# Optimization experiments

Measured on AMD Instinct MI355X. Metric: run time of the kernel, lower is better.

Reference implementation:

```python
import jax, jax.numpy as jnp
import numpy as np

N_NODES = 100000
N_EDGES = 1600000
D = 128
EPS = 0.0  # train_eps=False -> constant


def setup_inputs() -> dict:
    key = jax.random.key(0)
    k = jax.random.split(key, 6)
    s = 1.0 / np.sqrt(D)
    return {
        "X": jax.random.normal(k[0], (N_NODES, D), dtype=jnp.float32),
        "W1": jax.random.normal(k[1], (D, D), dtype=jnp.float32) * s,
        "b1": jnp.zeros((D,), dtype=jnp.float32),
        "W2": jax.random.normal(k[2], (D, D), dtype=jnp.float32) * s,
        "b2": jnp.zeros((D,), dtype=jnp.float32),
        "edge_src": jax.random.randint(k[3], (N_EDGES,), 0, N_NODES, dtype=jnp.int32),
        "edge_dst": jax.random.randint(k[4], (N_EDGES,), 0, N_NODES, dtype=jnp.int32),
    }


def reference(X, W1, b1, W2, b2, edge_src, edge_dst):
    # v2v sum aggregation: agg[i] = sum_{j in N(i)} X[j]
    msgs = X[edge_src]  # (E, D) gather
    agg = jax.ops.segment_sum(msgs, edge_dst, num_segments=N_NODES)  # (N, D)
    h = (1.0 + EPS) * X + agg
    # MLP: Linear -> ReLU -> Linear
    h = jax.nn.relu(h @ W1 + b1)
    out = h @ W2 + b2
    return out
```

## Files before the change

### kernel.cpp

```cpp
#include <hip/hip_runtime.h>
#include <hip/hip_bf16.h>

#define N_NODES 100000
#define N_EDGES 1600000
#define D 128

#define NBINS 196
#define BINSHIFT 9
#define BINCAP 10000
#define EPB 8192

typedef __bf16 bf16x8 __attribute__((ext_vector_type(8)));
typedef short short8 __attribute__((ext_vector_type(8)));
typedef float f32x4 __attribute__((ext_vector_type(4)));

__device__ __forceinline__ unsigned short f2bf(float f) {
  union { float f; unsigned u; } c; c.f = f;
  unsigned u = c.u;
  u += 0x7FFFu + ((u >> 16) & 1u);
  return (unsigned short)(u >> 16);
}
__device__ __forceinline__ float bflo(unsigned u) {
  union { unsigned u; float f; } c; c.u = u << 16; return c.f;
}
__device__ __forceinline__ float bfhi(unsigned u) {
  union { unsigned u; float f; } c; c.u = u & 0xFFFF0000u; return c.f;
}


__launch_bounds__(512)
__global__ void k_bin(const int* __restrict__ esrc, const int* __restrict__ edst,
                      int* __restrict__ g_bincnt, uint2* __restrict__ binbuf) {
  __shared__ int cnt[NBINS];
  __shared__ int base[NBINS];
  const int t = threadIdx.x;
  const int e0 = blockIdx.x * EPB;
  const int ne = min(EPB, N_EDGES - e0);
  for (int i = t; i < NBINS; i += 512) cnt[i] = 0;
  __syncthreads();
  for (int i = t; i < ne; i += 512)
    atomicAdd(&cnt[edst[e0 + i] >> BINSHIFT], 1);
  __syncthreads();
  for (int i = t; i < NBINS; i += 512) {
    base[i] = atomicAdd(&g_bincnt[i], cnt[i]);
    cnt[i] = 0;
  }
  __syncthreads();
  for (int i = t; i < ne; i += 512) {
    int d = edst[e0 + i];
    int s = esrc[e0 + i];
    int b = d >> BINSHIFT;
    int pos = base[b] + atomicAdd(&cnt[b], 1);
    binbuf[(size_t)b * BINCAP + pos] = make_uint2((unsigned)s, (unsigned)d);
  }
}

__global__ void k_binscan(const int* __restrict__ g_bincnt, int* __restrict__ binstart) {
  __shared__ int s[256];
  int t = threadIdx.x;
  int v = (t < NBINS) ? g_bincnt[t] : 0;
  s[t] = v;
  __syncthreads();
  for (int d = 1; d < 256; d <<= 1) {
    int x = (t >= d) ? s[t - d] : 0;
    __syncthreads();
    s[t] += x;
    __syncthreads();
  }
  if (t < NBINS) binstart[t] = s[t] - v;
}

__launch_bounds__(512)
__global__ void k_binsort(const uint2* __restrict__ binbuf, const int* __restrict__ g_bincnt,
                          const int* __restrict__ binstart, int* __restrict__ srt,
                          int* __restrict__ deg, int* __restrict__ offs) {
  __shared__ int hist[512];
  __shared__ int scan[512];
  const int b = blockIdx.x, t = threadIdx.x;
  const int cnt = g_bincnt[b];
  const int n0 = b << BINSHIFT;
  const int gbase = binstart[b];
  const uint2* eb = binbuf + (size_t)b * BINCAP;

  hist[t] = 0;
  __syncthreads();
  for (int i = t; i < cnt; i += 512)
    atomicAdd(&hist[eb[i].y - n0], 1);
  __syncthreads();
  int v = hist[t];
  scan[t] = v;
  __syncthreads();
  for (int d = 1; d < 512; d <<= 1) {
    int x = (t >= d) ? scan[t - d] : 0;
    __syncthreads();
    scan[t] += x;
    __syncthreads();
  }
  int n = n0 + t;
  if (n < N_NODES) {
    deg[n] = v;
    offs[n] = gbase + scan[t] - v;
  }
  hist[t] = scan[t] - v;
  __syncthreads();
  for (int i = t; i < cnt; i += 512) {
    uint2 e = eb[i];
    int pos = atomicAdd(&hist[e.y - n0], 1);
    srt[gbase + pos] = (int)e.x;
  }
}


__global__ void k_hist(const int* __restrict__ dst, int* __restrict__ deg) {
  int i = blockIdx.x * 256 + threadIdx.x;
  if (i < N_EDGES) atomicAdd(&deg[dst[i]], 1);
}

__global__ void k_scan1(const int* __restrict__ deg, int* __restrict__ offs,
                        int* __restrict__ bsum) {
  __shared__ int s[1024];
  int t = threadIdx.x;
  int i = blockIdx.x * 1024 + t;
  int v = (i < N_NODES) ? deg[i] : 0;
  s[t] = v;
  __syncthreads();
  for (int d = 1; d < 1024; d <<= 1) {
    int x = (t >= d) ? s[t - d] : 0;
    __syncthreads();
    s[t] += x;
    __syncthreads();
  }
  if (i < N_NODES) offs[i] = s[t] - v;
  if (t == 1023) bsum[blockIdx.x] = s[t];
}

__global__ void k_scan2(int* __restrict__ bsum) {
  __shared__ int s[128];
  int t = threadIdx.x;
  int v = (t < 98) ? bsum[t] : 0;
  s[t] = v;
  __syncthreads();
  for (int d = 1; d < 128; d <<= 1) {
    int x = (t >= d) ? s[t - d] : 0;
    __syncthreads();
    s[t] += x;
    __syncthreads();
  }
  if (t < 98) bsum[t] = s[t] - v;
}

__global__ void k_scan3(int* __restrict__ offs, const int* __restrict__ bsum) {
  int i = blockIdx.x * 1024 + threadIdx.x;
  if (i < N_NODES) offs[i] += bsum[blockIdx.x];
}

__global__ void k_bucket(const int* __restrict__ src, const int* __restrict__ dst,
                         int* __restrict__ offs, int* __restrict__ srt) {
  int i = blockIdx.x * 256 + threadIdx.x;
  if (i < N_EDGES) {
    int pos = atomicAdd(&offs[dst[i]], 1);
    srt[pos] = src[i];
  }
}

__global__ void k_cvt(const float* __restrict__ X, unsigned short* __restrict__ Xb) {
  size_t i = (size_t)(blockIdx.x * 256 + threadIdx.x) * 8;
  const float4* p = (const float4*)(X + i);
  float4 a = p[0], b = p[1];
  short8 s;
  s[0] = f2bf(a.x); s[1] = f2bf(a.y); s[2] = f2bf(a.z); s[3] = f2bf(a.w);
  s[4] = f2bf(b.x); s[5] = f2bf(b.y); s[6] = f2bf(b.z); s[7] = f2bf(b.w);
  *(short8*)(Xb + i) = s;
}

__global__ void k_gather_bf(const unsigned int* __restrict__ X1,
                            const int* __restrict__ deg, const int* __restrict__ offs,
                            const int* __restrict__ srt, unsigned int* __restrict__ h0) {
  int node = blockIdx.x * 4 + (threadIdx.x >> 6);
  int lane = threadIdx.x & 63;
  unsigned u = X1[(size_t)node * 64 + lane];
  float hx = bflo(u), hy = bfhi(u);
  int e = offs[node];
  int end = e + deg[node];
  for (; e + 8 <= end; e += 8) {
    int s0 = srt[e],     s1 = srt[e + 1], s2 = srt[e + 2], s3 = srt[e + 3];
    int s4 = srt[e + 4], s5 = srt[e + 5], s6 = srt[e + 6], s7 = srt[e + 7];
    unsigned u0 = X1[(size_t)s0 * 64 + lane];
    unsigned u1 = X1[(size_t)s1 * 64 + lane];
    unsigned u2 = X1[(size_t)s2 * 64 + lane];
    unsigned u3 = X1[(size_t)s3 * 64 + lane];
    unsigned u4 = X1[(size_t)s4 * 64 + lane];
    unsigned u5 = X1[(size_t)s5 * 64 + lane];
    unsigned u6 = X1[(size_t)s6 * 64 + lane];
    unsigned u7 = X1[(size_t)s7 * 64 + lane];
    hx += bflo(u0); hy += bfhi(u0);
    hx += bflo(u1); hy += bfhi(u1);
    hx += bflo(u2); hy += bfhi(u2);
    hx += bflo(u3); hy += bfhi(u3);
    hx += bflo(u4); hy += bfhi(u4);
    hx += bflo(u5); hy += bfhi(u5);
    hx += bflo(u6); hy += bfhi(u6);
    hx += bflo(u7); hy += bfhi(u7);
  }
  for (; e + 2 <= end; e += 2) {
    unsigned u0 = X1[(size_t)srt[e] * 64 + lane];
    unsigned u1 = X1[(size_t)srt[e + 1] * 64 + lane];
    hx += bflo(u0); hy += bfhi(u0);
    hx += bflo(u1); hy += bfhi(u1);
  }
  for (; e < end; ++e) {
    unsigned u0 = X1[(size_t)srt[e] * 64 + lane];
    hx += bflo(u0); hy += bfhi(u0);
  }
  h0[(size_t)node * 64 + lane] = ((unsigned)f2bf(hy) << 16) | f2bf(hx);
}

__global__ void k_gather(const float* __restrict__ X, const int* __restrict__ deg,
                         const int* __restrict__ offs, const int* __restrict__ srt,
                         float* __restrict__ out) {
  int node = blockIdx.x * 4 + (threadIdx.x >> 6);
  int lane = threadIdx.x & 63;
  const float2* X2 = (const float2*)X;
  float2 h = X2[(size_t)node * 64 + lane];
  int end = offs[node];
  int dg = deg[node];
  for (int e = end - dg; e < end; ++e) {
    int s = srt[e];
    float2 x = X2[(size_t)s * 64 + lane];
    h.x += x.x; h.y += x.y;
  }
  ((float2*)out)[(size_t)node * 64 + lane] = h;
}

#define BR 256
#define PADK 136

template <bool BF>
__launch_bounds__(512, 1)
__global__ void k_mlp(const void* __restrict__ h0v,
                      const float* __restrict__ W1, const float* __restrict__ b1,
                      const float* __restrict__ W2, const float* __restrict__ b2,
                      float* __restrict__ out) {
  __shared__ __attribute__((aligned(16))) unsigned short lW1[128 * PADK];
  __shared__ __attribute__((aligned(16))) unsigned short lW2[128 * PADK];
  __shared__ __attribute__((aligned(16))) unsigned short lH[BR * PADK];

  const int t = threadIdx.x;
  const int wave = t >> 6, lane = t & 63;
  const int lr = lane & 15, lg = lane >> 4;
  const int row0 = blockIdx.x * BR;
  const int wrow = row0 + wave * 32;

  for (int i = t; i < 128 * 128; i += 512) {
    int k = i >> 7, n = i & 127;
    lW1[n * PADK + k] = f2bf(W1[i]);
    lW2[n * PADK + k] = f2bf(W2[i]);
  }

  bf16x8 a[2][4];
#pragma unroll
  for (int tr = 0; tr < 2; ++tr) {
#pragma unroll
    for (int kb = 0; kb < 4; ++kb) {
      int r = wrow + tr * 16 + lr;
      if (r >= N_NODES) r = N_NODES - 1;
      if constexpr (BF) {
        const unsigned short* h0 = (const unsigned short*)h0v;
        a[tr][kb] = __builtin_bit_cast(bf16x8,
            *(const short8*)(h0 + (size_t)r * D + kb * 32 + lg * 8));
      } else {
        const float* h0 = (const float*)h0v;
        const float4* p = (const float4*)(h0 + (size_t)r * D + kb * 32 + lg * 8);
        float4 f0 = p[0], f1 = p[1];
        short8 s;
        s[0] = f2bf(f0.x); s[1] = f2bf(f0.y); s[2] = f2bf(f0.z); s[3] = f2bf(f0.w);
        s[4] = f2bf(f1.x); s[5] = f2bf(f1.y); s[6] = f2bf(f1.z); s[7] = f2bf(f1.w);
        a[tr][kb] = __builtin_bit_cast(bf16x8, s);
      }
    }
  }

  f32x4 acc[2][8];
#pragma unroll
  for (int nc = 0; nc < 8; ++nc) {
    float bb = b1[nc * 16 + lr];
#pragma unroll
    for (int tr = 0; tr < 2; ++tr) acc[tr][nc] = (f32x4){bb, bb, bb, bb};
  }

  __syncthreads();

#pragma unroll
  for (int nc = 0; nc < 8; ++nc) {
#pragma unroll
    for (int kb = 0; kb < 4; ++kb) {
      bf16x8 b = *(const bf16x8*)&lW1[(nc * 16 + lr) * PADK + kb * 32 + lg * 8];
#pragma unroll
      for (int tr = 0; tr < 2; ++tr)
        acc[tr][nc] = __builtin_amdgcn_mfma_f32_16x16x32_bf16(a[tr][kb], b, acc[tr][nc], 0, 0, 0);
    }
  }

#pragma unroll
  for (int tr = 0; tr < 2; ++tr) {
#pragma unroll
    for (int nc = 0; nc < 8; ++nc) {
#pragma unroll
      for (int r = 0; r < 4; ++r) {
        float v = acc[tr][nc][r];
        v = v > 0.f ? v : 0.f;
        int lrow = wave * 32 + tr * 16 + lg * 4 + r;
        lH[lrow * PADK + nc * 16 + lr] = f2bf(v);
      }
    }
  }

  __syncthreads();

  bf16x8 a2[2][4];
#pragma unroll
  for (int tr = 0; tr < 2; ++tr) {
#pragma unroll
    for (int kb = 0; kb < 4; ++kb)
      a2[tr][kb] = *(const bf16x8*)&lH[(wave * 32 + tr * 16 + lr) * PADK + kb * 32 + lg * 8];
  }

#pragma unroll
  for (int nc = 0; nc < 8; ++nc) {
    float bb = b2[nc * 16 + lr];
#pragma unroll
    for (int tr = 0; tr < 2; ++tr) acc[tr][nc] = (f32x4){bb, bb, bb, bb};
  }

#pragma unroll
  for (int nc = 0; nc < 8; ++nc) {
#pragma unroll
    for (int kb = 0; kb < 4; ++kb) {
      bf16x8 b = *(const bf16x8*)&lW2[(nc * 16 + lr) * PADK + kb * 32 + lg * 8];
#pragma unroll
      for (int tr = 0; tr < 2; ++tr)
        acc[tr][nc] = __builtin_amdgcn_mfma_f32_16x16x32_bf16(a2[tr][kb], b, acc[tr][nc], 0, 0, 0);
    }
  }

#pragma unroll
  for (int tr = 0; tr < 2; ++tr) {
#pragma unroll
    for (int nc = 0; nc < 8; ++nc) {
#pragma unroll
      for (int r = 0; r < 4; ++r) {
        int row = wrow + tr * 16 + lg * 4 + r;
        if (row < N_NODES) out[(size_t)row * D + nc * 16 + lr] = acc[tr][nc][r];
      }
    }
  }
}

extern "C" void kernel_launch(void* const* d_in, const int* in_sizes, int n_in,
                              void* d_out, int out_size, void* d_ws, size_t ws_size,
                              hipStream_t stream) {
  const float* X  = (const float*)d_in[0];
  const float* W1 = (const float*)d_in[1];
  const float* b1 = (const float*)d_in[2];
  const float* W2 = (const float*)d_in[3];
  const float* b2 = (const float*)d_in[4];
  const int* esrc = (const int*)d_in[5];
  const int* edst = (const int*)d_in[6];
  float* out = (float*)d_out;

  char* ws = (char*)d_ws;
  int* deg      = (int*)(ws);
  int* offs     = (int*)(ws + 400000);
  int* g_bincnt = (int*)(ws + 800000);
  int* binstart = (int*)(ws + 801024);
  int* srt      = (int*)(ws + 802048);
  unsigned short* Xb  = (unsigned short*)(ws + 7202048);
  unsigned short* h0b = (unsigned short*)(ws + 32802048);
  uint2* binbuf = (uint2*)(ws + 32802048);
  const size_t NEED = 58402048;

  if (ws_size >= NEED) {
    hipMemsetAsync(g_bincnt, 0, NBINS * sizeof(int), stream);
    k_cvt      <<<(N_NODES * D) / (256 * 8), 256, 0, stream>>>(X, Xb);
    k_bin      <<<(N_EDGES + EPB - 1) / EPB, 512, 0, stream>>>(esrc, edst, g_bincnt, binbuf);
    k_binscan  <<<1, 256, 0, stream>>>(g_bincnt, binstart);
    k_binsort  <<<NBINS, 512, 0, stream>>>(binbuf, g_bincnt, binstart, srt, deg, offs);
    k_gather_bf<<<N_NODES / 4, 256, 0, stream>>>((const unsigned*)Xb, deg, offs, srt,
                                                 (unsigned*)h0b);
    k_mlp<true><<<(N_NODES + BR - 1) / BR, 512, 0, stream>>>(h0b, W1, b1, W2, b2, out);
  } else {
    int* bsum = g_bincnt;
    hipMemsetAsync(deg, 0, N_NODES * sizeof(int), stream);
    k_hist  <<<N_EDGES / 256, 256, 0, stream>>>(edst, deg);
    k_scan1 <<<98, 1024, 0, stream>>>(deg, offs, bsum);
    k_scan2 <<<1, 128, 0, stream>>>(bsum);
    k_scan3 <<<98, 1024, 0, stream>>>(offs, bsum);
    k_bucket<<<N_EDGES / 256, 256, 0, stream>>>(esrc, edst, offs, srt);
    k_gather<<<N_NODES / 4, 256, 0, stream>>>(X, deg, offs, srt, out);
    k_mlp<false><<<(N_NODES + BR - 1) / BR, 512, 0, stream>>>(out, W1, b1, W2, b2, out);
  }
}
```

Measured before the change: 143.7 us.

## Fuse X conversion, weight pre-conversion and edge binning into one prep kernel

New measurement: 154.0 us. 7.1% more time.

```diff
diff --git a/kernel.cpp b/kernel.cpp
--- a/kernel.cpp
+++ b/kernel.cpp
@@ -9,6 +9,10 @@
 #define BINSHIFT 9
 #define BINCAP 10000
 #define EPB 8192
+
+#define PREP_CVT_BLOCKS 3125
+#define PREP_W_BLOCKS 8
+#define PREP_BIN_BLOCKS 196
 
 typedef __bf16 bf16x8 __attribute__((ext_vector_type(8)));
 typedef short short8 __attribute__((ext_vector_type(8)));
@@ -27,14 +31,44 @@
   union { unsigned u; float f; } c; c.u = u & 0xFFFF0000u; return c.f;
 }
 
+#define PADK 136
 
 __launch_bounds__(512)
-__global__ void k_bin(const int* __restrict__ esrc, const int* __restrict__ edst,
-                      int* __restrict__ g_bincnt, uint2* __restrict__ binbuf) {
+__global__ void k_prep(const float* __restrict__ X, unsigned short* __restrict__ Xb,
+                       const float* __restrict__ W1, const float* __restrict__ W2,
+                       unsigned short* __restrict__ Wimg,
+                       const int* __restrict__ esrc, const int* __restrict__ edst,
+                       int* __restrict__ g_bincnt, uint2* __restrict__ binbuf) {
   __shared__ int cnt[NBINS];
   __shared__ int base[NBINS];
-  const int t = threadIdx.x;
-  const int e0 = blockIdx.x * EPB;
+  const int b = blockIdx.x, t = threadIdx.x;
+
+  if (b < PREP_CVT_BLOCKS) {
+    size_t i = ((size_t)b * 512 + t) * 8;
+    const float4* p = (const float4*)(X + i);
+    float4 a = p[0], c = p[1];
+    short8 s;
+    s[0] = f2bf(a.x); s[1] = f2bf(a.y); s[2] = f2bf(a.z); s[3] = f2bf(a.w);
+    s[4] = f2bf(c.x); s[5] = f2bf(c.y); s[6] = f2bf(c.z); s[7] = f2bf(c.w);
+    *(short8*)(Xb + i) = s;
+    return;
+  }
+  if (b < PREP_CVT_BLOCKS + PREP_W_BLOCKS) {
+    int bb = b - PREP_CVT_BLOCKS;
+    const float* W = (bb & 4) ? W2 : W1;
+    unsigned short* img = Wimg + ((bb & 4) ? 128 * PADK : 0);
+    int k0 = (bb & 3) * 32;
+#pragma unroll
+    for (int it = 0; it < 8; ++it) {
+      int idx = it * 512 + t;
+      int k = k0 + (idx >> 7), n = idx & 127;
+      img[n * PADK + k] = f2bf(W[k * 128 + n]);
+    }
+    return;
+  }
+
+  const int eb = b - PREP_CVT_BLOCKS - PREP_W_BLOCKS;
+  const int e0 = eb * EPB;
   const int ne = min(EPB, N_EDGES - e0);
   for (int i = t; i < NBINS; i += 512) cnt[i] = 0;
   __syncthreads();
@@ -49,43 +83,39 @@
   for (int i = t; i < ne; i += 512) {
     int d = edst[e0 + i];
     int s = esrc[e0 + i];
-    int b = d >> BINSHIFT;
-    int pos = base[b] + atomicAdd(&cnt[b], 1);
-    binbuf[(size_t)b * BINCAP + pos] = make_uint2((unsigned)s, (unsigned)d);
-  }
-}
-
-__global__ void k_binscan(const int* __restrict__ g_bincnt, int* __restrict__ binstart) {
-  __shared__ int s[256];
-  int t = threadIdx.x;
-  int v = (t < NBINS) ? g_bincnt[t] : 0;
-  s[t] = v;
-  __syncthreads();
-  for (int d = 1; d < 256; d <<= 1) {
-    int x = (t >= d) ? s[t - d] : 0;
-    __syncthreads();
-    s[t] += x;
-    __syncthreads();
-  }
-  if (t < NBINS) binstart[t] = s[t] - v;
+    int bi = d >> BINSHIFT;
+    int pos = base[bi] + atomicAdd(&cnt[bi], 1);
+    binbuf[(size_t)bi * BINCAP + pos] = make_uint2((unsigned)s, (unsigned)d);
+  }
 }
 
 __launch_bounds__(512)
 __global__ void k_binsort(const uint2* __restrict__ binbuf, const int* __restrict__ g_bincnt,
-                          const int* __restrict__ binstart, int* __restrict__ srt,
-                          int* __restrict__ deg, int* __restrict__ offs) {
+                          int* __restrict__ srt, int* __restrict__ deg,
+                          int* __restrict__ offs) {
   __shared__ int hist[512];
   __shared__ int scan[512];
+  __shared__ int sb[256];
   const int b = blockIdx.x, t = threadIdx.x;
-  const int cnt = g_bincnt[b];
+
+  if (t < 256) sb[t] = (t < NBINS) ? g_bincnt[t] : 0;
+  __syncthreads();
+  for (int d = 1; d < 256; d <<= 1) {
+    int x = 0;
+    if (t < 256 && t >= d) x = sb[t - d];
+    __syncthreads();
+    if (t < 256) sb[t] += x;
+    __syncthreads();
+  }
+  const int cntb = g_bincnt[b];
+  const int gbase = (b == 0) ? 0 : sb[b - 1];
   const int n0 = b << BINSHIFT;
-  const int gbase = binstart[b];
-  const uint2* eb = binbuf + (size_t)b * BINCAP;
+  const uint2* ebuf = binbuf + (size_t)b * BINCAP;
 
   hist[t] = 0;
   __syncthreads();
-  for (int i = t; i < cnt; i += 512)
-    atomicAdd(&hist[eb[i].y - n0], 1);
+  for (int i = t; i < cntb; i += 512)
+    atomicAdd(&hist[ebuf[i].y - n0], 1);
   __syncthreads();
   int v = hist[t];
   scan[t] = v;
@@ -103,8 +133,8 @@
   }
   hist[t] = scan[t] - v;
   __syncthreads();
-  for (int i = t; i < cnt; i += 512) {
-    uint2 e = eb[i];
+  for (int i = t; i < cntb; i += 512) {
+    uint2 e = ebuf[i];
     int pos = atomicAdd(&hist[e.y - n0], 1);
     srt[gbase + pos] = (int)e.x;
   }
@@ -161,16 +191,6 @@
     int pos = atomicAdd(&offs[dst[i]], 1);
     srt[pos] = src[i];
   }
-}
-
-__global__ void k_cvt(const float* __restrict__ X, unsigned short* __restrict__ Xb) {
-  size_t i = (size_t)(blockIdx.x * 256 + threadIdx.x) * 8;
-  const float4* p = (const float4*)(X + i);
-  float4 a = p[0], b = p[1];
-  short8 s;
-  s[0] = f2bf(a.x); s[1] = f2bf(a.y); s[2] = f2bf(a.z); s[3] = f2bf(a.w);
-  s[4] = f2bf(b.x); s[5] = f2bf(b.y); s[6] = f2bf(b.z); s[7] = f2bf(b.w);
-  *(short8*)(Xb + i) = s;
 }
 
 __global__ void k_gather_bf(const unsigned int* __restrict__ X1,
@@ -233,16 +253,15 @@
 }
 
 #define BR 256
-#define PADK 136
 
 template <bool BF>
 __launch_bounds__(512, 1)
 __global__ void k_mlp(const void* __restrict__ h0v,
                       const float* __restrict__ W1, const float* __restrict__ b1,
                       const float* __restrict__ W2, const float* __restrict__ b2,
+                      const unsigned short* __restrict__ Wimg,
                       float* __restrict__ out) {
-  __shared__ __attribute__((aligned(16))) unsigned short lW1[128 * PADK];
-  __shared__ __attribute__((aligned(16))) unsigned short lW2[128 * PADK];
+  __shared__ __attribute__((aligned(16))) unsigned short lW[2 * 128 * PADK];
   __shared__ __attribute__((aligned(16))) unsigned short lH[BR * PADK];
 
   const int t = threadIdx.x;
@@ -251,10 +270,16 @@
   const int row0 = blockIdx.x * BR;
   const int wrow = row0 + wave * 32;
 
-  for (int i = t; i < 128 * 128; i += 512) {
-    int k = i >> 7, n = i & 127;
-    lW1[n * PADK + k] = f2bf(W1[i]);
-    lW2[n * PADK + k] = f2bf(W2[i]);
+  if constexpr (BF) {
+    const uint4* wi = (const uint4*)Wimg;
+    for (int i = t; i < (2 * 128 * PADK * 2) / 16; i += 512)
+      ((uint4*)lW)[i] = wi[i];
+  } else {
+    for (int i = t; i < 128 * 128; i += 512) {
+      int k = i >> 7, n = i & 127;
+      lW[n * PADK + k] = f2bf(W1[i]);
+      lW[128 * PADK + n * PADK + k] = f2bf(W2[i]);
+    }
   }
 
   bf16x8 a[2][4];
@@ -294,7 +319,7 @@
   for (int nc = 0; nc < 8; ++nc) {
 #pragma unroll
     for (int kb = 0; kb < 4; ++kb) {
-      bf16x8 b = *(const bf16x8*)&lW1[(nc * 16 + lr) * PADK + kb * 32 + lg * 8];
+      bf16x8 b = *(const bf16x8*)&lW[(nc * 16 + lr) * PADK + kb * 32 + lg * 8];
 #pragma unroll
       for (int tr = 0; tr < 2; ++tr)
         acc[tr][nc] = __builtin_amdgcn_mfma_f32_16x16x32_bf16(a[tr][kb], b, acc[tr][nc], 0, 0, 0);
@@ -336,7 +361,7 @@
   for (int nc = 0; nc < 8; ++nc) {
 #pragma unroll
     for (int kb = 0; kb < 4; ++kb) {
-      bf16x8 b = *(const bf16x8*)&lW2[(nc * 16 + lr) * PADK + kb * 32 + lg * 8];
+      bf16x8 b = *(const bf16x8*)&lW[128 * PADK + (nc * 16 + lr) * PADK + kb * 32 + lg * 8];
 #pragma unroll
       for (int tr = 0; tr < 2; ++tr)
         acc[tr][nc] = __builtin_amdgcn_mfma_f32_16x16x32_bf16(a2[tr][kb], b, acc[tr][nc], 0, 0, 0);
@@ -372,22 +397,21 @@
   int* deg      = (int*)(ws);
   int* offs     = (int*)(ws + 400000);
   int* g_bincnt = (int*)(ws + 800000);
-  int* binstart = (int*)(ws + 801024);
   int* srt      = (int*)(ws + 802048);
   unsigned short* Xb  = (unsigned short*)(ws + 7202048);
   unsigned short* h0b = (unsigned short*)(ws + 32802048);
   uint2* binbuf = (uint2*)(ws + 32802048);
-  const size_t NEED = 58402048;
+  unsigned short* Wimg = (unsigned short*)(ws + 58402048);
+  const size_t NEED = 58471680;
 
   if (ws_size >= NEED) {
     hipMemsetAsync(g_bincnt, 0, NBINS * sizeof(int), stream);
-    k_cvt      <<<(N_NODES * D) / (256 * 8), 256, 0, stream>>>(X, Xb);
-    k_bin      <<<(N_EDGES + EPB - 1) / EPB, 512, 0, stream>>>(esrc, edst, g_bincnt, binbuf);
-    k_binscan  <<<1, 256, 0, stream>>>(g_bincnt, binstart);
-    k_binsort  <<<NBINS, 512, 0, stream>>>(binbuf, g_bincnt, binstart, srt, deg, offs);
+    k_prep<<<PREP_CVT_BLOCKS + PREP_W_BLOCKS + PREP_BIN_BLOCKS, 512, 0, stream>>>(
+        X, Xb, W1, W2, Wimg, esrc, edst, g_bincnt, binbuf);
+    k_binsort<<<NBINS, 512, 0, stream>>>(binbuf, g_bincnt, srt, deg, offs);
     k_gather_bf<<<N_NODES / 4, 256, 0, stream>>>((const unsigned*)Xb, deg, offs, srt,
                                                  (unsigned*)h0b);
-    k_mlp<true><<<(N_NODES + BR - 1) / BR, 512, 0, stream>>>(h0b, W1, b1, W2, b2, out);
+    k_mlp<true><<<(N_NODES + BR - 1) / BR, 512, 0, stream>>>(h0b, W1, b1, W2, b2, Wimg, out);
   } else {
     int* bsum = g_bincnt;
     hipMemsetAsync(deg, 0, N_NODES * sizeof(int), stream);
@@ -397,6 +421,6 @@
     k_scan3 <<<98, 1024, 0, stream>>>(offs, bsum);
     k_bucket<<<N_EDGES / 256, 256, 0, stream>>>(esrc, edst, offs, srt);
     k_gather<<<N_NODES / 4, 256, 0, stream>>>(X, deg, offs, srt, out);
-    k_mlp<false><<<(N_NODES + BR - 1) / BR, 512, 0, stream>>>(out, W1, b1, W2, b2, out);
-  }
-}
+    k_mlp<false><<<(N_NODES + BR - 1) / BR, 512, 0, stream>>>(out, W1, b1, W2, b2, nullptr, out);
+  }
+}
```
